# Optimization experiments

Hardware: AMD Instinct MI355X
Metric: run time of the kernel (lower is better)

The kernel has to match this reference:

```python
import math
import jax, jax.numpy as jnp
import numpy as np

EMBED_DIM = 1024
NUM_HEADS = 16
HEAD_DIM = EMBED_DIM // NUM_HEADS
ROTARY_DIM = HEAD_DIM  # default: rotary_dim = head_dim
BASE = 10000.0


def _rope_cos_sin(seq_len, d, dtype=jnp.float32):
    # theta: [d/2], positions: [S]
    theta = 1.0 / (BASE ** (jnp.arange(0, d, 2, dtype=jnp.float32) / d))
    pos = jnp.arange(seq_len, dtype=jnp.float32)
    idx_theta = pos[:, None] * theta[None, :]          # [S, d/2]
    idx_theta2 = jnp.concatenate([idx_theta, idx_theta], axis=-1)  # [S, d]
    return jnp.cos(idx_theta2).astype(dtype), jnp.sin(idx_theta2).astype(dtype)


def _apply_rope(x):
    # x: [B, H, S, head_dim]; rotate first ROTARY_DIM features
    S = x.shape[-2]
    cos, sin = _rope_cos_sin(S, ROTARY_DIM, x.dtype)   # [S, ROTARY_DIM]
    x_rope, x_pass = x[..., :ROTARY_DIM], x[..., ROTARY_DIM:]
    d2 = ROTARY_DIM // 2
    neg_half = jnp.concatenate([-x_rope[..., d2:], x_rope[..., :d2]], axis=-1)
    x_rope = x_rope * cos + neg_half * sin
    return jnp.concatenate([x_rope, x_pass], axis=-1)


def setup_inputs() -> dict:
    key = jax.random.key(0)
    ks = jax.random.split(key, 9)
    B, S, E = 4, 2048, EMBED_DIM
    scale = 1.0 / math.sqrt(E)
    inp = {
        "x": jax.random.normal(ks[0], (B, S, E), dtype=jnp.float32),
        "attn_mask": jnp.ones((B, S), dtype=jnp.int32),
        "Wq": jax.random.normal(ks[1], (E, E), dtype=jnp.float32) * scale,
        "bq": jnp.zeros((E,), dtype=jnp.float32),
        "Wk": jax.random.normal(ks[2], (E, E), dtype=jnp.float32) * scale,
        "bk": jnp.zeros((E,), dtype=jnp.float32),
        "Wv": jax.random.normal(ks[3], (E, E), dtype=jnp.float32) * scale,
        "bv": jnp.zeros((E,), dtype=jnp.float32),
        "Wo": jax.random.normal(ks[4], (E, E), dtype=jnp.float32) * scale,
        "bo": jnp.zeros((E,), dtype=jnp.float32),
    }
    return inp


def reference(x, attn_mask, Wq, bq, Wk, bk, Wv, bv, Wo, bo):
    B, S, E = x.shape
    H, D = NUM_HEADS, HEAD_DIM

    def proj(W, b):
        # [B,S,E] -> [B,H,S,D]
        y = jnp.einsum('bse,ef->bsf', x, W) + b
        return y.reshape(B, S, H, D).transpose(0, 2, 1, 3)

    q = _apply_rope(proj(Wq, bq))
    k = _apply_rope(proj(Wk, bk))
    v = proj(Wv, bv)

    scores = jnp.einsum('bhsd,bhtd->bhst', q, k) / math.sqrt(D)  # [B,H,S,S]
    mask = attn_mask[:, None, None, :]  # [B,1,1,S]
    scores = jnp.where(mask == 0, jnp.float32(-1e9).astype(scores.dtype), scores)
    attn = jax.nn.softmax(scores, axis=-1)
    out = jnp.einsum('bhst,bhtd->bhsd', attn, v)  # [B,H,S,D]
    out = out.transpose(0, 2, 1, 3).reshape(B, S, E)
    return jnp.einsum('bse,ef->bsf', out, Wo) + bo
```

## Files before the change

kernel.cpp:

```cpp
#include <hip/hip_runtime.h>
#include <math.h>

typedef __attribute__((ext_vector_type(8))) short short8;
typedef __attribute__((ext_vector_type(4))) float f32x4;
typedef __attribute__((ext_vector_type(4))) unsigned short us4;
typedef __attribute__((ext_vector_type(4))) unsigned int u32x4;
typedef __attribute__((ext_vector_type(4))) int i32x4;
typedef unsigned short u16;
typedef unsigned int u32;

#define LOG2E 1.4426950408889634f

static __device__ __forceinline__ u16 f2bf(float f){
  u32 u = __builtin_bit_cast(u32, f);
  u = (u + 0x7FFFu + ((u >> 16) & 1u)) >> 16;
  return (u16)u;
}

static __device__ __forceinline__ void gload16(const void* g, void* l){
  __builtin_amdgcn_global_load_lds((const __attribute__((address_space(1))) void*)g,
                                   (__attribute__((address_space(3))) void*)l,
                                   16, 0, 0);
}

static __device__ __forceinline__ f32x4 mfma16(short8 a, short8 b, f32x4 c){
  return __builtin_amdgcn_mfma_f32_16x16x32_bf16(a, b, c, 0, 0, 0);
}

__global__ void rope_tab_k(float* __restrict__ cosT, float* __restrict__ sinT){
  int idx = blockIdx.x * 256 + threadIdx.x;
  int s = idx >> 5, i = idx & 31;
  double th = pow(10000.0, -((double)(2 * i)) / 64.0);
  float ang = (float)s * (float)th;
  cosT[idx] = (float)cos((double)ang);
  sinT[idx] = (float)sin((double)ang);
}

__global__ void cvt_x_k(const float* __restrict__ x, u16* __restrict__ xb, int n){
  int i = (blockIdx.x * 256 + threadIdx.x) * 4;
  if (i >= n) return;
  f32x4 v = *(const f32x4*)(x + i);
  us4 o; o[0]=f2bf(v[0]); o[1]=f2bf(v[1]); o[2]=f2bf(v[2]); o[3]=f2bf(v[3]);
  *(us4*)(xb + i) = o;
}

__global__ void wt_cvt_k(const float* __restrict__ W0, const float* __restrict__ W1,
                         const float* __restrict__ W2, const float* __restrict__ W3,
                         u16* __restrict__ out){
  __shared__ float t[32][33];
  const float* W = (blockIdx.z == 0) ? W0 : (blockIdx.z == 1) ? W1 : (blockIdx.z == 2) ? W2 : W3;
  u16* O = out + (size_t)blockIdx.z * 1024 * 1024;
  int tx = threadIdx.x, ty = threadIdx.y;
  int kb = blockIdx.y * 32, nb = blockIdx.x * 32;
  #pragma unroll
  for (int i = 0; i < 4; i++)
    t[ty + i*8][tx] = W[(size_t)(kb + ty + i*8) * 1024 + nb + tx];
  __syncthreads();
  #pragma unroll
  for (int i = 0; i < 4; i++)
    O[(size_t)(nb + ty + i*8) * 1024 + kb + tx] = f2bf(t[tx][ty + i*8]);
}

__global__ __launch_bounds__(256, 2)
void qkv_gemm_k(const u16* __restrict__ A, const u16* __restrict__ WT,
                const float* __restrict__ bq, const float* __restrict__ bk,
                const float* __restrict__ bv,
                const float* __restrict__ cosT, const float* __restrict__ sinT,
                u16* __restrict__ Qr, u16* __restrict__ Kr, u16* __restrict__ Vt)
{
  __shared__ __align__(16) u16 Al[128][64];
  __shared__ __align__(16) u16 Bl[128][64];
  const int mode = blockIdx.y >> 3;
  const int cy   = blockIdx.y & 7;
  const u16* BT = WT + (size_t)mode * 1024 * 1024;
  const float* bias = (mode == 0) ? bq : (mode == 1) ? bk : bv;
  u16* outB = (mode == 0) ? Qr : (mode == 1) ? Kr : Vt;

  const int tid = threadIdx.x;
  const int w = tid >> 6, lane = tid & 63, g = lane >> 4, c = lane & 15;
  const int wr = w >> 1, wc = w & 1;
  const int R0 = blockIdx.x * 128, C0 = cy * 128;

  f32x4 acc[4][4];
  const f32x4 vz = {0.f, 0.f, 0.f, 0.f};
  #pragma unroll
  for (int mi = 0; mi < 4; mi++)
    #pragma unroll
    for (int ni = 0; ni < 4; ni++) acc[mi][ni] = vz;

  const u16* gA[4]; const u16* gB[4]; u16* lA[4]; u16* lB[4];
  #pragma unroll
  for (int i = 0; i < 4; i++){
    int I = w * 4 + i;
    int rr = I * 8 + (lane >> 3), kk = (lane & 7) * 8;
    gA[i] = A  + (size_t)(R0 + rr) * 1024 + kk;
    gB[i] = BT + (size_t)(C0 + rr) * 1024 + kk;
    lA[i] = &Al[I * 8][0];
    lB[i] = &Bl[I * 8][0];
  }

  for (int t = 0; t < 16; ++t){
    const int k0 = t * 64;
    #pragma unroll
    for (int i = 0; i < 4; i++){
      gload16(gA[i] + k0, lA[i]);
      gload16(gB[i] + k0, lB[i]);
    }
    __syncthreads();
    #pragma unroll
    for (int ki = 0; ki < 2; ++ki){
      short8 af[4], bfr[4];
      #pragma unroll
      for (int mi = 0; mi < 4; mi++) af[mi]  = *(const short8*)&Al[wr*64 + mi*16 + c][ki*32 + g*8];
      #pragma unroll
      for (int ni = 0; ni < 4; ni++) bfr[ni] = *(const short8*)&Bl[wc*64 + ni*16 + c][ki*32 + g*8];
      #pragma unroll
      for (int mi = 0; mi < 4; mi++)
        #pragma unroll
        for (int ni = 0; ni < 4; ni++)
          acc[mi][ni] = mfma16(af[mi], bfr[ni], acc[mi][ni]);
    }
    __syncthreads();
  }

  if (mode == 2){
    int h = cy * 2 + wc;
    #pragma unroll
    for (int ni = 0; ni < 4; ni++){
      int col = C0 + wc*64 + ni*16 + c;
      int d = ni*16 + c;
      float bvv = bias[col];
      #pragma unroll
      for (int mi = 0; mi < 4; mi++){
        int row0 = R0 + wr*64 + mi*16 + g*4;
        int b = row0 >> 11, s0 = row0 & 2047;
        us4 pk;
        #pragma unroll
        for (int r = 0; r < 4; r++) pk[r] = f2bf(acc[mi][ni][r] + bvv);
        *(us4*)&outB[((size_t)(b*16 + h)*64 + d)*2048 + s0] = pk;
      }
    }
  } else {
    int h = cy * 2 + wc;
    const float qs = (mode == 0) ? 0.125f : 1.0f;
    float bvv[4];
    #pragma unroll
    for (int ni = 0; ni < 4; ni++) bvv[ni] = bias[C0 + wc*64 + ni*16 + c];
    #pragma unroll
    for (int mi = 0; mi < 4; mi++){
      int row0 = R0 + wr*64 + mi*16 + g*4;
      int b = row0 >> 11;
      #pragma unroll
      for (int r = 0; r < 4; r++){
        int s = (row0 + r) & 2047;
        float v0 = acc[mi][0][r] + bvv[0];
        float v1 = acc[mi][1][r] + bvv[1];
        float v2 = acc[mi][2][r] + bvv[2];
        float v3 = acc[mi][3][r] + bvv[3];
        float ca = cosT[s*32 + c],      sa = sinT[s*32 + c];
        float cb = cosT[s*32 + 16 + c], sb = sinT[s*32 + 16 + c];
        float o0 = (v0*ca - v2*sa) * qs, o2 = (v2*ca + v0*sa) * qs;
        float o1 = (v1*cb - v3*sb) * qs, o3 = (v3*cb + v1*sb) * qs;
        size_t base = ((size_t)(b*16 + h)*2048 + s)*64;
        outB[base +  0 + c] = f2bf(o0);
        outB[base + 16 + c] = f2bf(o1);
        outB[base + 32 + c] = f2bf(o2);
        outB[base + 48 + c] = f2bf(o3);
      }
    }
  }
}

__global__ __launch_bounds__(256, 2)
void out_gemm_k(const u16* __restrict__ A, const u16* __restrict__ BT,
                const float* __restrict__ bias, float* __restrict__ outF)
{
  __shared__ __align__(16) u16 Al[128][64];
  __shared__ __align__(16) u16 Bl[128][64];
  const int tid = threadIdx.x;
  const int w = tid >> 6, lane = tid & 63, g = lane >> 4, c = lane & 15;
  const int wr = w >> 1, wc = w & 1;
  const int R0 = blockIdx.x * 128, C0 = blockIdx.y * 128;

  f32x4 acc[4][4];
  const f32x4 vz = {0.f, 0.f, 0.f, 0.f};
  #pragma unroll
  for (int mi = 0; mi < 4; mi++)
    #pragma unroll
    for (int ni = 0; ni < 4; ni++) acc[mi][ni] = vz;

  const u16* gA[4]; const u16* gB[4]; u16* lA[4]; u16* lB[4];
  #pragma unroll
  for (int i = 0; i < 4; i++){
    int I = w * 4 + i;
    int rr = I * 8 + (lane >> 3), kk = (lane & 7) * 8;
    gA[i] = A  + (size_t)(R0 + rr) * 1024 + kk;
    gB[i] = BT + (size_t)(C0 + rr) * 1024 + kk;
    lA[i] = &Al[I * 8][0];
    lB[i] = &Bl[I * 8][0];
  }

  for (int t = 0; t < 16; ++t){
    const int k0 = t * 64;
    #pragma unroll
    for (int i = 0; i < 4; i++){
      gload16(gA[i] + k0, lA[i]);
      gload16(gB[i] + k0, lB[i]);
    }
    __syncthreads();
    #pragma unroll
    for (int ki = 0; ki < 2; ++ki){
      short8 af[4], bfr[4];
      #pragma unroll
      for (int mi = 0; mi < 4; mi++) af[mi]  = *(const short8*)&Al[wr*64 + mi*16 + c][ki*32 + g*8];
      #pragma unroll
      for (int ni = 0; ni < 4; ni++) bfr[ni] = *(const short8*)&Bl[wc*64 + ni*16 + c][ki*32 + g*8];
      #pragma unroll
      for (int mi = 0; mi < 4; mi++)
        #pragma unroll
        for (int ni = 0; ni < 4; ni++)
          acc[mi][ni] = mfma16(af[mi], bfr[ni], acc[mi][ni]);
    }
    __syncthreads();
  }

  #pragma unroll
  for (int mi = 0; mi < 4; mi++){
    #pragma unroll
    for (int ni = 0; ni < 4; ni++){
      int col = C0 + wc*64 + ni*16 + c;
      float bvv = bias[col];
      int row0 = R0 + wr*64 + mi*16 + g*4;
      #pragma unroll
      for (int r = 0; r < 4; r++)
        outF[(size_t)(row0 + r) * 1024 + col] = acc[mi][ni][r] + bvv;
    }
  }
}

__global__ __launch_bounds__(512, 6)
void attn_fwd_k(const u16* __restrict__ Q, const u16* __restrict__ K, const u16* __restrict__ V,
                const int* __restrict__ msk, u16* __restrict__ AO)
{
  __shared__ __align__(16) u16 Kl[2][64][64];
  __shared__ __align__(16) u16 Vl[2][64][64];
  __shared__ __align__(8) unsigned char Ml[2048];
  const int tid = threadIdx.x;
  const int w = tid >> 6, lane = tid & 63, g = lane >> 4, c = lane & 15;

  const int lin = blockIdx.y * 16 + blockIdx.x;
  const int v_  = (lin & 7) * 128 + (lin >> 3);
  const int bh = v_ >> 4, b = bh >> 4, h = bh & 15;
  const int qw = (v_ & 15) * 128 + w * 16;

  short8 qb[2];
  #pragma unroll
  for (int ki = 0; ki < 2; ki++)
    qb[ki] = *(const short8*)&Q[((size_t)bh*2048 + qw + c)*64 + ki*32 + g*8];

  const int l3 = lane >> 3, l7 = lane & 7;
  const int scol = (l7 ^ l3) * 8;
  const int s8 = w*8 + l3;
  const int ps = (s8 & 0x20) | ((s8 & 0x10) >> 2) | ((s8 & 0x0C) << 1) | (s8 & 3);
  const u16* gK = K + ((size_t)bh*2048 + ps)*64 + scol;
  const u16* gV = V + ((size_t)bh*64 + s8)*2048 + scol;

  gload16(gK, &Kl[0][w*8][0]);
  gload16(gV, &Vl[0][w*8][0]);

  {
    const int* mp = msk + b*2048 + tid*4;
    i32x4 a = *(const i32x4*)mp;
    u32 lo = (a[0] ? 1u : 0u) | (a[1] ? 0x100u : 0u) | (a[2] ? 0x10000u : 0u) | (a[3] ? 0x1000000u : 0u);
    *(u32*)&Ml[tid*4] = lo;
  }
  asm volatile("s_waitcnt lgkmcnt(0)" ::: "memory");

  f32x4 oacc[4];
  float mrun = -1e30f, lrun = 0.f;
  const f32x4 vz = {0.f, 0.f, 0.f, 0.f};
  #pragma unroll
  for (int nd = 0; nd < 4; nd++) oacc[nd] = vz;

  const int cs0 = (g*8) ^ ((c & 7) << 3);
  const int cs1 = (32 + g*8) ^ ((c & 7) << 3);

  for (int t = 0; t < 32; ++t){
    gload16(gK + (size_t)(t+1) * 64 * 64, &Kl[(t+1)&1][w*8][0]);
    gload16(gV + (size_t)(t+1) * 64,      &Vl[(t+1)&1][w*8][0]);
    asm volatile("s_waitcnt vmcnt(2)" ::: "memory");
    __builtin_amdgcn_s_barrier();
    asm volatile("" ::: "memory");

    const u16* Kb = &Kl[t&1][0][0];
    const u16* Vb = &Vl[t&1][0][0];
    const int t0 = t * 64;

    f32x4 sacc[4];
    #pragma unroll
    for (int nt = 0; nt < 4; nt++) sacc[nt] = vz;
    #pragma unroll
    for (int ki = 0; ki < 2; ki++){
      const int cs = ki ? cs1 : cs0;
      short8 ka[4];
      #pragma unroll
      for (int nt = 0; nt < 4; nt++) ka[nt] = *(const short8*)&Kb[(nt*16 + c)*64 + cs];
      #pragma unroll
      for (int nt = 0; nt < 4; nt++)
        sacc[nt] = mfma16(ka[nt], qb[ki], sacc[nt]);
    }

    {
      const u32 mw0 = *(const u32*)&Ml[t0 + 8*g];
      const u32 mw1 = *(const u32*)&Ml[t0 + 8*g + 4];
      const u32 mw2 = *(const u32*)&Ml[t0 + 32 + 8*g];
      const u32 mw3 = *(const u32*)&Ml[t0 + 32 + 8*g + 4];
      if (!__all((mw0 & mw1 & mw2 & mw3) == 0x01010101u)){
        const u32 mw[4] = {mw0, mw1, mw2, mw3};
        #pragma unroll
        for (int nt = 0; nt < 4; nt++)
          #pragma unroll
          for (int r = 0; r < 4; r++)
            if (((mw[nt] >> (8*r)) & 0xFFu) == 0) sacc[nt][r] = -1e9f;
      }
    }

    float a0 = fmaxf(fmaxf(sacc[0][0], sacc[0][1]), fmaxf(sacc[0][2], sacc[0][3]));
    float a1 = fmaxf(fmaxf(sacc[1][0], sacc[1][1]), fmaxf(sacc[1][2], sacc[1][3]));
    float a2 = fmaxf(fmaxf(sacc[2][0], sacc[2][1]), fmaxf(sacc[2][2], sacc[2][3]));
    float a3 = fmaxf(fmaxf(sacc[3][0], sacc[3][1]), fmaxf(sacc[3][2], sacc[3][3]));
    float pm = fmaxf(fmaxf(a0, a1), fmaxf(a2, a3));
    pm = fmaxf(pm, __shfl_xor(pm, 16, 64));
    pm = fmaxf(pm, __shfl_xor(pm, 32, 64));

    if (__any(pm > mrun + 8.f)){
      float mn = fmaxf(mrun, pm);
      float al = exp2f((mrun - mn) * LOG2E);
      mrun = mn;
      lrun *= al;
      float b0 = __shfl(al, g*4 + 0, 64);
      float b1 = __shfl(al, g*4 + 1, 64);
      float b2 = __shfl(al, g*4 + 2, 64);
      float b3 = __shfl(al, g*4 + 3, 64);
      #pragma unroll
      for (int nd = 0; nd < 4; nd++){
        oacc[nd][0] *= b0; oacc[nd][1] *= b1;
        oacc[nd][2] *= b2; oacc[nd][3] *= b3;
      }
    }

    short8 pa[2];
    {
      const float nm = -mrun * LOG2E;
      float p[16]; u32 rb[16];
      #pragma unroll
      for (int nt = 0; nt < 4; nt++)
        #pragma unroll
        for (int r = 0; r < 4; r++){
          float pp = exp2f(fmaf(sacc[nt][r], LOG2E, nm));
          p[nt*4 + r] = pp;
          u32 u = __builtin_bit_cast(u32, pp);
          rb[nt*4 + r] = u + 0x7FFFu + ((u >> 16) & 1u);
        }
      float s0 = (p[0] + p[1]) + (p[2] + p[3]);
      float s1 = (p[4] + p[5]) + (p[6] + p[7]);
      float s2 = (p[8] + p[9]) + (p[10] + p[11]);
      float s3 = (p[12] + p[13]) + (p[14] + p[15]);
      lrun += (s0 + s1) + (s2 + s3);
      u32x4 q0 = { __builtin_amdgcn_perm(rb[1],  rb[0],  0x07060302u),
                   __builtin_amdgcn_perm(rb[3],  rb[2],  0x07060302u),
                   __builtin_amdgcn_perm(rb[5],  rb[4],  0x07060302u),
                   __builtin_amdgcn_perm(rb[7],  rb[6],  0x07060302u) };
      u32x4 q1 = { __builtin_amdgcn_perm(rb[9],  rb[8],  0x07060302u),
                   __builtin_amdgcn_perm(rb[11], rb[10], 0x07060302u),
                   __builtin_amdgcn_perm(rb[13], rb[12], 0x07060302u),
                   __builtin_amdgcn_perm(rb[15], rb[14], 0x07060302u) };
      pa[0] = __builtin_bit_cast(short8, q0);
      pa[1] = __builtin_bit_cast(short8, q1);
    }

    #pragma unroll
    for (int ki = 0; ki < 2; ki++){
      const int cs = ki ? cs1 : cs0;
      short8 va[4];
      #pragma unroll
      for (int nd = 0; nd < 4; nd++) va[nd] = *(const short8*)&Vb[(nd*16 + c)*64 + cs];
      #pragma unroll
      for (int nd = 0; nd < 4; nd++)
        oacc[nd] = mfma16(pa[ki], va[nd], oacc[nd]);
    }

    asm volatile("" ::: "memory");
    __builtin_amdgcn_s_barrier();
    asm volatile("" ::: "memory");
  }

  lrun += __shfl_xor(lrun, 16, 64);
  lrun += __shfl_xor(lrun, 32, 64);
  #pragma unroll
  for (int r = 0; r < 4; r++){
    float li = __shfl(lrun, g*4 + r, 64);
    float inv = 1.0f / li;
    int q = qw + g*4 + r;
    size_t base = ((size_t)b*2048 + q)*1024 + h*64;
    #pragma unroll
    for (int nd = 0; nd < 4; nd++)
      AO[base + nd*16 + c] = f2bf(oacc[nd][r] * inv);
  }
}

extern "C" void kernel_launch(void* const* d_in, const int* in_sizes, int n_in,
                              void* d_out, int out_size, void* d_ws, size_t ws_size,
                              hipStream_t stream)
{
  const float* x  = (const float*)d_in[0];
  const int* mask = (const int*)d_in[1];
  const float* Wq = (const float*)d_in[2];
  const float* bq = (const float*)d_in[3];
  const float* Wk = (const float*)d_in[4];
  const float* bk = (const float*)d_in[5];
  const float* Wv = (const float*)d_in[6];
  const float* bv = (const float*)d_in[7];
  const float* Wo = (const float*)d_in[8];
  const float* bo = (const float*)d_in[9];
  float* out = (float*)d_out;
  (void)in_sizes; (void)n_in; (void)out_size; (void)ws_size;

  char* ws = (char*)d_ws;
  size_t off = 0;
  auto alloc = [&](size_t bytes){ void* p = ws + off; off += (bytes + 255) & ~(size_t)255; return p; };
  u16* xb    = (u16*)alloc((size_t)8192 * 1024 * 2);
  u16* WT    = (u16*)alloc((size_t)4 * 1024 * 1024 * 2);
  float* cosT = (float*)alloc((size_t)2048 * 32 * 4);
  float* sinT = (float*)alloc((size_t)2048 * 32 * 4);
  u16* Qr    = (u16*)alloc((size_t)8192 * 1024 * 2);
  u16* Kr    = (u16*)alloc((size_t)8192 * 1024 * 2);
  u16* Vt    = (u16*)alloc((size_t)8192 * 1024 * 2);
  u16* AO    = (u16*)alloc((size_t)8192 * 1024 * 2);

  rope_tab_k<<<dim3(256), dim3(256), 0, stream>>>(cosT, sinT);
  cvt_x_k<<<dim3(8192), dim3(256), 0, stream>>>(x, xb, 8192 * 1024);
  wt_cvt_k<<<dim3(32, 32, 4), dim3(32, 8), 0, stream>>>(Wq, Wk, Wv, Wo, WT);

  qkv_gemm_k<<<dim3(64, 24), dim3(256), 0, stream>>>(xb, WT, bq, bk, bv, cosT, sinT, Qr, Kr, Vt);

  attn_fwd_k<<<dim3(16, 64), dim3(512), 0, stream>>>(Qr, Kr, Vt, mask, AO);

  out_gemm_k<<<dim3(64, 8), dim3(256), 0, stream>>>(AO, WT + 3*1024*1024, bo, out);
}
```

Baseline: 254.3 us.

## Double KV tile to 128 per barrier step in attention kernel

The attention loop now stages 128 keys and values per iteration instead of 64, halving the number of barrier and wait steps and issuing two async global-to-LDS loads per tensor per thread. The V tile uses a new 128-wide XOR swizzle and K gets an extra row offset. LDS use doubles and the launch-bounds occupancy hint drops from 6 to 4 blocks, trading latency hiding for fewer synchronisations.

Result: faster. 245.6 us (-3.4%).

```diff
diff --git a/kernel.cpp b/kernel.cpp
--- a/kernel.cpp
+++ b/kernel.cpp
@@ -238,12 +238,12 @@
   }
 }
 
-__global__ __launch_bounds__(512, 6)
+__global__ __launch_bounds__(512, 4)
 void attn_fwd_k(const u16* __restrict__ Q, const u16* __restrict__ K, const u16* __restrict__ V,
                 const int* __restrict__ msk, u16* __restrict__ AO)
 {
-  __shared__ __align__(16) u16 Kl[2][64][64];
-  __shared__ __align__(16) u16 Vl[2][64][64];
+  __shared__ __align__(16) u16 Kl[2][128][64];
+  __shared__ __align__(16) u16 Vl[2][64][128];
   __shared__ __align__(8) unsigned char Ml[2048];
   const int tid = threadIdx.x;
   const int w = tid >> 6, lane = tid & 63, g = lane >> 4, c = lane & 15;
@@ -259,14 +259,27 @@
     qb[ki] = *(const short8*)&Q[((size_t)bh*2048 + qw + c)*64 + ki*32 + g*8];
 
   const int l3 = lane >> 3, l7 = lane & 7;
-  const int scol = (l7 ^ l3) * 8;
-  const int s8 = w*8 + l3;
-  const int ps = (s8 & 0x20) | ((s8 & 0x10) >> 2) | ((s8 & 0x0C) << 1) | (s8 & 3);
-  const u16* gK = K + ((size_t)bh*2048 + ps)*64 + scol;
-  const u16* gV = V + ((size_t)bh*64 + s8)*2048 + scol;
-
-  gload16(gK, &Kl[0][w*8][0]);
-  gload16(gV, &Vl[0][w*8][0]);
+  const int kcol = (l7 ^ l3) * 8;
+  const u16* gKs[2];
+  #pragma unroll
+  for (int j = 0; j < 2; j++){
+    int sr = w*16 + j*8 + l3;
+    int s = sr & 63;
+    int ps = (s & 0x20) | ((s & 0x10) >> 2) | ((s & 0x0C) << 1) | (s & 3);
+    gKs[j] = K + ((size_t)bh*2048 + (sr & 64) + ps)*64 + kcol;
+  }
+  const u16* gVs[2];
+  #pragma unroll
+  for (int j = 0; j < 2; j++){
+    int vr = w*8 + j*4 + (lane >> 4);
+    int lc = (lane & 15) ^ (vr & 15);
+    gVs[j] = V + ((size_t)bh*64 + vr)*2048 + lc*8;
+  }
+
+  #pragma unroll
+  for (int j = 0; j < 2; j++) gload16(gKs[j], &Kl[0][w*16 + j*8][0]);
+  #pragma unroll
+  for (int j = 0; j < 2; j++) gload16(gVs[j], &Vl[0][w*8 + j*4][0]);
 
   {
     const int* mp = msk + b*2048 + tid*4;
@@ -282,112 +295,120 @@
   #pragma unroll
   for (int nd = 0; nd < 4; nd++) oacc[nd] = vz;
 
-  const int cs0 = (g*8) ^ ((c & 7) << 3);
-  const int cs1 = (32 + g*8) ^ ((c & 7) << 3);
-
-  for (int t = 0; t < 32; ++t){
-    gload16(gK + (size_t)(t+1) * 64 * 64, &Kl[(t+1)&1][w*8][0]);
-    gload16(gV + (size_t)(t+1) * 64,      &Vl[(t+1)&1][w*8][0]);
-    asm volatile("s_waitcnt vmcnt(2)" ::: "memory");
+  for (int t = 0; t < 16; ++t){
+    {
+      const size_t ko = (size_t)(t+1) * 128 * 64;
+      const size_t vo = (size_t)(t+1) * 128;
+      #pragma unroll
+      for (int j = 0; j < 2; j++) gload16(gKs[j] + ko, &Kl[(t+1)&1][w*16 + j*8][0]);
+      #pragma unroll
+      for (int j = 0; j < 2; j++) gload16(gVs[j] + vo, &Vl[(t+1)&1][w*8 + j*4][0]);
+    }
+    asm volatile("s_waitcnt vmcnt(4)" ::: "memory");
     __builtin_amdgcn_s_barrier();
     asm volatile("" ::: "memory");
 
     const u16* Kb = &Kl[t&1][0][0];
     const u16* Vb = &Vl[t&1][0][0];
-    const int t0 = t * 64;
-
-    f32x4 sacc[4];
-    #pragma unroll
-    for (int nt = 0; nt < 4; nt++) sacc[nt] = vz;
-    #pragma unroll
-    for (int ki = 0; ki < 2; ki++){
-      const int cs = ki ? cs1 : cs0;
-      short8 ka[4];
-      #pragma unroll
-      for (int nt = 0; nt < 4; nt++) ka[nt] = *(const short8*)&Kb[(nt*16 + c)*64 + cs];
-      #pragma unroll
-      for (int nt = 0; nt < 4; nt++)
-        sacc[nt] = mfma16(ka[nt], qb[ki], sacc[nt]);
-    }
-
-    {
-      const u32 mw0 = *(const u32*)&Ml[t0 + 8*g];
-      const u32 mw1 = *(const u32*)&Ml[t0 + 8*g + 4];
-      const u32 mw2 = *(const u32*)&Ml[t0 + 32 + 8*g];
-      const u32 mw3 = *(const u32*)&Ml[t0 + 32 + 8*g + 4];
-      if (!__all((mw0 & mw1 & mw2 & mw3) == 0x01010101u)){
-        const u32 mw[4] = {mw0, mw1, mw2, mw3};
+
+    #pragma unroll
+    for (int half = 0; half < 2; ++half){
+      const int t0 = t * 128 + half * 64;
+
+      f32x4 sacc[4];
+      #pragma unroll
+      for (int nt = 0; nt < 4; nt++) sacc[nt] = vz;
+      #pragma unroll
+      for (int ki = 0; ki < 2; ki++){
+        const int cs = (((ki*4 + g) ^ (c & 7)) * 8);
+        short8 ka[4];
+        #pragma unroll
+        for (int nt = 0; nt < 4; nt++)
+          ka[nt] = *(const short8*)&Kb[(half*64 + nt*16 + c)*64 + cs];
+        #pragma unroll
+        for (int nt = 0; nt < 4; nt++)
+          sacc[nt] = mfma16(ka[nt], qb[ki], sacc[nt]);
+      }
+
+      {
+        const u32 mw0 = *(const u32*)&Ml[t0 + 8*g];
+        const u32 mw1 = *(const u32*)&Ml[t0 + 8*g + 4];
+        const u32 mw2 = *(const u32*)&Ml[t0 + 32 + 8*g];
+        const u32 mw3 = *(const u32*)&Ml[t0 + 32 + 8*g + 4];
+        if (!__all((mw0 & mw1 & mw2 & mw3) == 0x01010101u)){
+          const u32 mw[4] = {mw0, mw1, mw2, mw3};
+          #pragma unroll
+          for (int nt = 0; nt < 4; nt++)
+            #pragma unroll
+            for (int r = 0; r < 4; r++)
+              if (((mw[nt] >> (8*r)) & 0xFFu) == 0) sacc[nt][r] = -1e9f;
+        }
+      }
+
+      float a0 = fmaxf(fmaxf(sacc[0][0], sacc[0][1]), fmaxf(sacc[0][2], sacc[0][3]));
+      float a1 = fmaxf(fmaxf(sacc[1][0], sacc[1][1]), fmaxf(sacc[1][2], sacc[1][3]));
+      float a2 = fmaxf(fmaxf(sacc[2][0], sacc[2][1]), fmaxf(sacc[2][2], sacc[2][3]));
+      float a3 = fmaxf(fmaxf(sacc[3][0], sacc[3][1]), fmaxf(sacc[3][2], sacc[3][3]));
+      float pm = fmaxf(fmaxf(a0, a1), fmaxf(a2, a3));
+      pm = fmaxf(pm, __shfl_xor(pm, 16, 64));
+      pm = fmaxf(pm, __shfl_xor(pm, 32, 64));
+
+      if (__any(pm > mrun + 8.f)){
+        float mn = fmaxf(mrun, pm);
+        float al = exp2f((mrun - mn) * LOG2E);
+        mrun = mn;
+        lrun *= al;
+        float b0 = __shfl(al, g*4 + 0, 64);
+        float b1 = __shfl(al, g*4 + 1, 64);
+        float b2 = __shfl(al, g*4 + 2, 64);
+        float b3 = __shfl(al, g*4 + 3, 64);
+        #pragma unroll
+        for (int nd = 0; nd < 4; nd++){
+          oacc[nd][0] *= b0; oacc[nd][1] *= b1;
+          oacc[nd][2] *= b2; oacc[nd][3] *= b3;
+        }
+      }
+
+      short8 pa[2];
+      {
+        const float nm = -mrun * LOG2E;
+        float p[16]; u32 rb[16];
         #pragma unroll
         for (int nt = 0; nt < 4; nt++)
           #pragma unroll
-          for (int r = 0; r < 4; r++)
-            if (((mw[nt] >> (8*r)) & 0xFFu) == 0) sacc[nt][r] = -1e9f;
-      }
-    }
-
-    float a0 = fmaxf(fmaxf(sacc[0][0], sacc[0][1]), fmaxf(sacc[0][2], sacc[0][3]));
-    float a1 = fmaxf(fmaxf(sacc[1][0], sacc[1][1]), fmaxf(sacc[1][2], sacc[1][3]));
-    float a2 = fmaxf(fmaxf(sacc[2][0], sacc[2][1]), fmaxf(sacc[2][2], sacc[2][3]));
-    float a3 = fmaxf(fmaxf(sacc[3][0], sacc[3][1]), fmaxf(sacc[3][2], sacc[3][3]));
-    float pm = fmaxf(fmaxf(a0, a1), fmaxf(a2, a3));
-    pm = fmaxf(pm, __shfl_xor(pm, 16, 64));
-    pm = fmaxf(pm, __shfl_xor(pm, 32, 64));
-
-    if (__any(pm > mrun + 8.f)){
-      float mn = fmaxf(mrun, pm);
-      float al = exp2f((mrun - mn) * LOG2E);
-      mrun = mn;
-      lrun *= al;
-      float b0 = __shfl(al, g*4 + 0, 64);
-      float b1 = __shfl(al, g*4 + 1, 64);
-      float b2 = __shfl(al, g*4 + 2, 64);
-      float b3 = __shfl(al, g*4 + 3, 64);
-      #pragma unroll
-      for (int nd = 0; nd < 4; nd++){
-        oacc[nd][0] *= b0; oacc[nd][1] *= b1;
-        oacc[nd][2] *= b2; oacc[nd][3] *= b3;
-      }
-    }
-
-    short8 pa[2];
-    {
-      const float nm = -mrun * LOG2E;
-      float p[16]; u32 rb[16];
-      #pragma unroll
-      for (int nt = 0; nt < 4; nt++)
-        #pragma unroll
-        for (int r = 0; r < 4; r++){
-          float pp = exp2f(fmaf(sacc[nt][r], LOG2E, nm));
-          p[nt*4 + r] = pp;
-          u32 u = __builtin_bit_cast(u32, pp);
-          rb[nt*4 + r] = u + 0x7FFFu + ((u >> 16) & 1u);
-        }
-      float s0 = (p[0] + p[1]) + (p[2] + p[3]);
-      float s1 = (p[4] + p[5]) + (p[6] + p[7]);
-      float s2 = (p[8] + p[9]) + (p[10] + p[11]);
-      float s3 = (p[12] + p[13]) + (p[14] + p[15]);
-      lrun += (s0 + s1) + (s2 + s3);
-      u32x4 q0 = { __builtin_amdgcn_perm(rb[1],  rb[0],  0x07060302u),
-                   __builtin_amdgcn_perm(rb[3],  rb[2],  0x07060302u),
-                   __builtin_amdgcn_perm(rb[5],  rb[4],  0x07060302u),
-                   __builtin_amdgcn_perm(rb[7],  rb[6],  0x07060302u) };
-      u32x4 q1 = { __builtin_amdgcn_perm(rb[9],  rb[8],  0x07060302u),
-                   __builtin_amdgcn_perm(rb[11], rb[10], 0x07060302u),
-                   __builtin_amdgcn_perm(rb[13], rb[12], 0x07060302u),
-                   __builtin_amdgcn_perm(rb[15], rb[14], 0x07060302u) };
-      pa[0] = __builtin_bit_cast(short8, q0);
-      pa[1] = __builtin_bit_cast(short8, q1);
-    }
-
-    #pragma unroll
-    for (int ki = 0; ki < 2; ki++){
-      const int cs = ki ? cs1 : cs0;
-      short8 va[4];
-      #pragma unroll
-      for (int nd = 0; nd < 4; nd++) va[nd] = *(const short8*)&Vb[(nd*16 + c)*64 + cs];
-      #pragma unroll
-      for (int nd = 0; nd < 4; nd++)
-        oacc[nd] = mfma16(pa[ki], va[nd], oacc[nd]);
+          for (int r = 0; r < 4; r++){
+            float pp = exp2f(fmaf(sacc[nt][r], LOG2E, nm));
+            p[nt*4 + r] = pp;
+            u32 u = __builtin_bit_cast(u32, pp);
+            rb[nt*4 + r] = u + 0x7FFFu + ((u >> 16) & 1u);
+          }
+        float s0 = (p[0] + p[1]) + (p[2] + p[3]);
+        float s1 = (p[4] + p[5]) + (p[6] + p[7]);
+        float s2 = (p[8] + p[9]) + (p[10] + p[11]);
+        float s3 = (p[12] + p[13]) + (p[14] + p[15]);
+        lrun += (s0 + s1) + (s2 + s3);
+        u32x4 q0 = { __builtin_amdgcn_perm(rb[1],  rb[0],  0x07060302u),
+                     __builtin_amdgcn_perm(rb[3],  rb[2],  0x07060302u),
+                     __builtin_amdgcn_perm(rb[5],  rb[4],  0x07060302u),
+                     __builtin_amdgcn_perm(rb[7],  rb[6],  0x07060302u) };
+        u32x4 q1 = { __builtin_amdgcn_perm(rb[9],  rb[8],  0x07060302u),
+                     __builtin_amdgcn_perm(rb[11], rb[10], 0x07060302u),
+                     __builtin_amdgcn_perm(rb[13], rb[12], 0x07060302u),
+                     __builtin_amdgcn_perm(rb[15], rb[14], 0x07060302u) };
+        pa[0] = __builtin_bit_cast(short8, q0);
+        pa[1] = __builtin_bit_cast(short8, q1);
+      }
+
+      #pragma unroll
+      for (int ki = 0; ki < 2; ki++){
+        short8 va[4];
+        #pragma unroll
+        for (int nd = 0; nd < 4; nd++)
+          va[nd] = *(const short8*)&Vb[(nd*16 + c)*128 + (((half*8 + ki*4 + g) ^ c) * 8)];
+        #pragma unroll
+        for (int nd = 0; nd < 4; nd++)
+          oacc[nd] = mfma16(pa[ki], va[nd], oacc[nd]);
+      }
     }
 
     asm volatile("" ::: "memory");
```
